# Kernel tuning notes

Measured on AMD Instinct MI355X. Metric: run time of the kernel, lower is better.

The kernel has to match this reference:

```python
import jax, jax.numpy as jnp
import numpy as np

N_NODES = 100000
N_EDGES = 1200000
IN_F = 64
OUT_F = 64


def setup_inputs() -> dict:
    key = jax.random.key(0)
    ks = jax.random.split(key, 8)
    rows = jax.random.randint(ks[0], (N_EDGES,), 0, N_NODES)
    cols = jax.random.randint(ks[1], (N_EDGES,), 0, N_NODES)
    vals = jax.random.uniform(ks[2], (N_EDGES,), dtype=jnp.float32)
    features = jax.random.normal(ks[3], (N_NODES, IN_F), dtype=jnp.float32)
    W1 = jax.random.normal(ks[4], (IN_F, OUT_F), dtype=jnp.float32) / np.sqrt(IN_F)
    b1 = jax.random.normal(ks[5], (OUT_F,), dtype=jnp.float32) * 0.01
    W2 = jax.random.normal(ks[6], (IN_F, OUT_F), dtype=jnp.float32) / np.sqrt(IN_F)
    b2 = jax.random.normal(ks[7], (OUT_F,), dtype=jnp.float32) * 0.01
    return {"rows": rows, "cols": cols, "vals": vals, "features": features,
            "W1": W1, "b1": b1, "W2": W2, "b2": b2}


def _spmm(rows, cols, vals, x):
    # y[r] = sum_{e: rows[e]==r} vals[e] * x[cols[e]]  -- COO SpMM via gather + segment_sum
    msgs = vals[:, None] * x[cols]  # [E, F]
    return jax.ops.segment_sum(msgs, rows, num_segments=N_NODES)


def reference(rows, cols, vals, features, W1, b1, W2, b2):
    # L1 = laplacian + selfLoop(identity)  =>  L1 @ X = L @ X + X
    agg1 = _spmm(rows, cols, vals, features) + features          # [N, inF]
    inter_feature = features * features                           # elementwise square
    agg2 = _spmm(rows, cols, vals, inter_feature)                 # [N, inF]
    part1 = agg1 @ W1 + b1                                        # linear
    part2 = agg2 @ W2 + b2                                        # interActTransform
    return part1 + part2
```

## Files before the change

kernel.cpp:

```cpp
#include <hip/hip_runtime.h>


#define ROWS_PER_BUCKET 128
#define ROW_SHIFT 7
#define NBUCK_PAD 784
#define SCAN_T 196
#define CAP 2048
#define CHUNK 4096
#define MAXB 2048
#define COL_BITS 17
#define COL_MASK 0x1FFFF
#define OVF_CAP 65536

__device__ __forceinline__ unsigned short f2bf(float x) {
    unsigned u = __float_as_uint(x);
    unsigned r = (u + 0x7FFFu + ((u >> 16) & 1u)) >> 16;
    return (unsigned short)r;
}
__device__ __forceinline__ float bf2f(unsigned short h) {
    return __uint_as_float(((unsigned)h) << 16);
}

__global__ __launch_bounds__(256) void node_transform(
    const float* __restrict__ X, const float* __restrict__ W1,
    const float* __restrict__ b1, const float* __restrict__ W2,
    const float* __restrict__ b2, unsigned short* __restrict__ Yb,
    float* __restrict__ Z, int n_nodes)
{
    __shared__ float W1s[64 * 64];
    __shared__ float W2s[64 * 64];
    __shared__ float xs[128][65];
    __shared__ float bs[64];

    const int tid = threadIdx.x;
    const int base = blockIdx.x * 128;

    {
        const float4* w1v = (const float4*)W1;
        const float4* w2v = (const float4*)W2;
        float4* s1 = (float4*)W1s;
        float4* s2 = (float4*)W2s;
#pragma unroll
        for (int i = 0; i < 4; ++i) {
            s1[tid + 256 * i] = w1v[tid + 256 * i];
            s2[tid + 256 * i] = w2v[tid + 256 * i];
        }
    }
    if (tid < 64) bs[tid] = b1[tid] + b2[tid];

    {
#pragma unroll
        for (int i = 0; i < 8; ++i) {
            int idx = (tid + 256 * i) * 4;
            int r = idx >> 6, c = idx & 63;
            if (base + r < n_nodes) {
                float4 v = *(const float4*)(X + (size_t)base * 64 + idx);
                xs[r][c + 0] = v.x; xs[r][c + 1] = v.y;
                xs[r][c + 2] = v.z; xs[r][c + 3] = v.w;
            }
        }
    }
    __syncthreads();

    const int tx = tid & 7;
    const int ty = tid >> 3;

    float acc1[4][8] = {};
    float acc2[4][8] = {};

#pragma unroll 2
    for (int k = 0; k < 64; ++k) {
        float4 wa0 = *(const float4*)(W1s + k * 64 + tx * 8);
        float4 wa1 = *(const float4*)(W1s + k * 64 + tx * 8 + 4);
        float4 wb0 = *(const float4*)(W2s + k * 64 + tx * 8);
        float4 wb1 = *(const float4*)(W2s + k * 64 + tx * 8 + 4);
#pragma unroll
        for (int i = 0; i < 4; ++i) {
            float xv = xs[ty * 4 + i][k];
            float xq = xv * xv;
            acc1[i][0] = fmaf(xv, wa0.x, acc1[i][0]);
            acc1[i][1] = fmaf(xv, wa0.y, acc1[i][1]);
            acc1[i][2] = fmaf(xv, wa0.z, acc1[i][2]);
            acc1[i][3] = fmaf(xv, wa0.w, acc1[i][3]);
            acc1[i][4] = fmaf(xv, wa1.x, acc1[i][4]);
            acc1[i][5] = fmaf(xv, wa1.y, acc1[i][5]);
            acc1[i][6] = fmaf(xv, wa1.z, acc1[i][6]);
            acc1[i][7] = fmaf(xv, wa1.w, acc1[i][7]);
            acc2[i][0] = fmaf(xq, wb0.x, acc2[i][0]);
            acc2[i][1] = fmaf(xq, wb0.y, acc2[i][1]);
            acc2[i][2] = fmaf(xq, wb0.z, acc2[i][2]);
            acc2[i][3] = fmaf(xq, wb0.w, acc2[i][3]);
            acc2[i][4] = fmaf(xq, wb1.x, acc2[i][4]);
            acc2[i][5] = fmaf(xq, wb1.y, acc2[i][5]);
            acc2[i][6] = fmaf(xq, wb1.z, acc2[i][6]);
            acc2[i][7] = fmaf(xq, wb1.w, acc2[i][7]);
        }
    }

    float bv[8];
#pragma unroll
    for (int j = 0; j < 8; ++j) bv[j] = bs[tx * 8 + j];

#pragma unroll
    for (int i = 0; i < 4; ++i) {
        int node = base + ty * 4 + i;
        if (node < n_nodes) {
            float z[8];
            unsigned pk[4];
#pragma unroll
            for (int j = 0; j < 4; ++j) {
                float ylo = acc1[i][2 * j]     + acc2[i][2 * j];
                float yhi = acc1[i][2 * j + 1] + acc2[i][2 * j + 1];
                pk[j] = (unsigned)f2bf(ylo) | ((unsigned)f2bf(yhi) << 16);
            }
#pragma unroll
            for (int j = 0; j < 8; ++j) z[j] = acc1[i][j] + bv[j];
            unsigned short* yp = Yb + (size_t)node * 64 + tx * 8;
            float* zp = Z + (size_t)node * 64 + tx * 8;
            *(uint4*)(yp) = make_uint4(pk[0], pk[1], pk[2], pk[3]);
            *(float4*)(zp)     = make_float4(z[0], z[1], z[2], z[3]);
            *(float4*)(zp + 4) = make_float4(z[4], z[5], z[6], z[7]);
        }
    }
}


__global__ __launch_bounds__(256) void cursor_init(
    int* __restrict__ gcursor, int* __restrict__ ovf_count, int nbp) {
    int i = blockIdx.x * 256 + threadIdx.x;
    if (i < nbp) gcursor[i] = i * CAP;
    if (i == 0) *ovf_count = 0;
}

__global__ __launch_bounds__(256) void bin_scatter(
    const int* __restrict__ rows, const int* __restrict__ cols,
    const float* __restrict__ vals, int* __restrict__ gcursor,
    int2* __restrict__ packed, int* __restrict__ ovf_count,
    int4* __restrict__ ovf, int n_edges) {
    __shared__ int lcount[NBUCK_PAD];
    __shared__ int lstart[NBUCK_PAD];
    __shared__ int lcursor[NBUCK_PAD];
    __shared__ int gbase[NBUCK_PAD];
    __shared__ int sx[CHUNK];
    __shared__ int sy[CHUNK];
    __shared__ unsigned short sbk[CHUNK];

    int tid = threadIdx.x;
    int eb0 = blockIdx.x * CHUNK;
    int cnt = min(CHUNK, n_edges - eb0);

    for (int k = tid; k < NBUCK_PAD; k += 256) lcount[k] = 0;
    __syncthreads();

    for (int i = tid; i < cnt; i += 256)
        atomicAdd(&lcount[rows[eb0 + i] >> ROW_SHIFT], 1);
    __syncthreads();

    int c0 = 0, c1 = 0, c2 = 0, c3 = 0, psum = 0;
    if (tid < SCAN_T) {
        c0 = lcount[tid * 4 + 0]; c1 = lcount[tid * 4 + 1];
        c2 = lcount[tid * 4 + 2]; c3 = lcount[tid * 4 + 3];
        psum = c0 + c1 + c2 + c3;
    }
    sx[tid] = psum;
    __syncthreads();
#pragma unroll
    for (int o = 1; o < 256; o <<= 1) {
        int t = (tid >= o) ? sx[tid - o] : 0;
        __syncthreads();
        sx[tid] += t;
        __syncthreads();
    }
    int base0 = sx[tid] - psum;
    __syncthreads();
    if (tid < SCAN_T) {
        lstart[tid * 4 + 0] = base0;
        lstart[tid * 4 + 1] = base0 + c0;
        lstart[tid * 4 + 2] = base0 + c0 + c1;
        lstart[tid * 4 + 3] = base0 + c0 + c1 + c2;
    }
    __syncthreads();

    for (int k = tid; k < NBUCK_PAD; k += 256) {
        lcursor[k] = lstart[k];
        if (lcount[k] > 0) gbase[k] = atomicAdd(&gcursor[k], lcount[k]);
    }
    __syncthreads();

    for (int i = tid; i < cnt; i += 256) {
        int r = rows[eb0 + i];
        int b = r >> ROW_SHIFT;
        int p = atomicAdd(&lcursor[b], 1);
        sx[p] = ((r & (ROWS_PER_BUCKET - 1)) << COL_BITS) | cols[eb0 + i];
        sy[p] = __float_as_int(vals[eb0 + i]);
        sbk[p] = (unsigned short)b;
    }
    __syncthreads();

    for (int i = tid; i < cnt; i += 256) {
        int b = sbk[i];
        int dest = gbase[b] + (i - lstart[b]);
        if (dest < (b + 1) * CAP) {
            packed[dest] = make_int2(sx[i], sy[i]);
        } else {
            int p = atomicAdd(ovf_count, 1);
            if (p < OVF_CAP)
                ovf[p] = make_int4(b * ROWS_PER_BUCKET + (sx[i] >> COL_BITS),
                                   sx[i] & COL_MASK, sy[i], 0);
        }
    }
}

__global__ __launch_bounds__(256) void bucket_gather_rows(
    const int* __restrict__ gcursor, const int2* __restrict__ packed,
    const unsigned short* __restrict__ Yb, float* __restrict__ out,
    int n_nodes) {
    __shared__ int2 sxy[MAXB];
    __shared__ int hist[ROWS_PER_BUCKET];
    __shared__ int chs[ROWS_PER_BUCKET];
    __shared__ int chc[ROWS_PER_BUCKET];

    int tid = threadIdx.x;
    int bucket = blockIdx.x >> 1;
    int rhalf = (blockIdx.x & 1) * 64;
    int fpair = tid & 31;
    int rowlane = tid >> 5;
    int s = bucket * CAP;
    int e = min(gcursor[bucket], s + CAP);
    int row0 = bucket * ROWS_PER_BUCKET;
    const unsigned* __restrict__ Y32 = (const unsigned*)Yb;

    for (int cb = s; cb < e; cb += MAXB) {
        int cnt = min(MAXB, e - cb);

        if (tid < ROWS_PER_BUCKET) hist[tid] = 0;
        __syncthreads();

        for (int i = tid; i < cnt; i += 256)
            atomicAdd(&hist[packed[cb + i].x >> COL_BITS], 1);
        __syncthreads();

        if (tid < ROWS_PER_BUCKET) chs[tid] = hist[tid];
        __syncthreads();
#pragma unroll
        for (int o = 1; o < ROWS_PER_BUCKET; o <<= 1) {
            int t = 0;
            if (tid < ROWS_PER_BUCKET && tid >= o) t = chs[tid - o];
            __syncthreads();
            if (tid < ROWS_PER_BUCKET) chs[tid] += t;
            __syncthreads();
        }
        if (tid < ROWS_PER_BUCKET) {
            int excl = chs[tid] - hist[tid];
            chs[tid] = excl;
            chc[tid] = excl;
        }
        __syncthreads();

        for (int i = tid; i < cnt; i += 256) {
            int2 a = packed[cb + i];
            int p = atomicAdd(&chc[a.x >> COL_BITS], 1);
            sxy[p] = a;
        }
        __syncthreads();

        for (int rr = 0; rr < 8; ++rr) {
            int r = rhalf + rowlane * 8 + rr;
            int rc = hist[r];
            int node = row0 + r;
            if (rc == 0 || node >= n_nodes) continue;
            int rs = chs[r];
            float a0 = 0.f, a1 = 0.f;
            int j = 0;
            for (; j + 8 <= rc; j += 8) {
                int2 e0 = sxy[rs + j + 0], e1 = sxy[rs + j + 1];
                int2 e2 = sxy[rs + j + 2], e3 = sxy[rs + j + 3];
                int2 e4 = sxy[rs + j + 4], e5 = sxy[rs + j + 5];
                int2 e6 = sxy[rs + j + 6], e7 = sxy[rs + j + 7];
                unsigned u0 = Y32[(size_t)(e0.x & COL_MASK) * 32 + fpair];
                unsigned u1 = Y32[(size_t)(e1.x & COL_MASK) * 32 + fpair];
                unsigned u2 = Y32[(size_t)(e2.x & COL_MASK) * 32 + fpair];
                unsigned u3 = Y32[(size_t)(e3.x & COL_MASK) * 32 + fpair];
                unsigned u4 = Y32[(size_t)(e4.x & COL_MASK) * 32 + fpair];
                unsigned u5 = Y32[(size_t)(e5.x & COL_MASK) * 32 + fpair];
                unsigned u6 = Y32[(size_t)(e6.x & COL_MASK) * 32 + fpair];
                unsigned u7 = Y32[(size_t)(e7.x & COL_MASK) * 32 + fpair];
                float v0 = __int_as_float(e0.y), v1 = __int_as_float(e1.y);
                float v2 = __int_as_float(e2.y), v3 = __int_as_float(e3.y);
                float v4 = __int_as_float(e4.y), v5 = __int_as_float(e5.y);
                float v6 = __int_as_float(e6.y), v7 = __int_as_float(e7.y);
                a0 = fmaf(v0, __uint_as_float(u0 << 16), a0);
                a1 = fmaf(v0, __uint_as_float(u0 & 0xFFFF0000u), a1);
                a0 = fmaf(v1, __uint_as_float(u1 << 16), a0);
                a1 = fmaf(v1, __uint_as_float(u1 & 0xFFFF0000u), a1);
                a0 = fmaf(v2, __uint_as_float(u2 << 16), a0);
                a1 = fmaf(v2, __uint_as_float(u2 & 0xFFFF0000u), a1);
                a0 = fmaf(v3, __uint_as_float(u3 << 16), a0);
                a1 = fmaf(v3, __uint_as_float(u3 & 0xFFFF0000u), a1);
                a0 = fmaf(v4, __uint_as_float(u4 << 16), a0);
                a1 = fmaf(v4, __uint_as_float(u4 & 0xFFFF0000u), a1);
                a0 = fmaf(v5, __uint_as_float(u5 << 16), a0);
                a1 = fmaf(v5, __uint_as_float(u5 & 0xFFFF0000u), a1);
                a0 = fmaf(v6, __uint_as_float(u6 << 16), a0);
                a1 = fmaf(v6, __uint_as_float(u6 & 0xFFFF0000u), a1);
                a0 = fmaf(v7, __uint_as_float(u7 << 16), a0);
                a1 = fmaf(v7, __uint_as_float(u7 & 0xFFFF0000u), a1);
            }
            for (; j + 2 <= rc; j += 2) {
                int2 e0 = sxy[rs + j + 0], e1 = sxy[rs + j + 1];
                unsigned u0 = Y32[(size_t)(e0.x & COL_MASK) * 32 + fpair];
                unsigned u1 = Y32[(size_t)(e1.x & COL_MASK) * 32 + fpair];
                float v0 = __int_as_float(e0.y), v1 = __int_as_float(e1.y);
                a0 = fmaf(v0, __uint_as_float(u0 << 16), a0);
                a1 = fmaf(v0, __uint_as_float(u0 & 0xFFFF0000u), a1);
                a0 = fmaf(v1, __uint_as_float(u1 << 16), a0);
                a1 = fmaf(v1, __uint_as_float(u1 & 0xFFFF0000u), a1);
            }
            if (j < rc) {
                int2 e0 = sxy[rs + j];
                unsigned u0 = Y32[(size_t)(e0.x & COL_MASK) * 32 + fpair];
                float v0 = __int_as_float(e0.y);
                a0 = fmaf(v0, __uint_as_float(u0 << 16), a0);
                a1 = fmaf(v0, __uint_as_float(u0 & 0xFFFF0000u), a1);
            }
            float2* op = (float2*)(out + (size_t)node * 64 + fpair * 2);
            float2 o = *op;
            o.x += a0; o.y += a1;
            *op = o;
        }
        __syncthreads();
    }
}

__global__ __launch_bounds__(256) void overflow_scatter(
    const int* __restrict__ ovf_count, const int4* __restrict__ ovf,
    const unsigned short* __restrict__ Yb, float* __restrict__ out) {
    int cnt = min(*ovf_count, OVF_CAP);
    long long total = (long long)cnt * 64;
    for (long long i = blockIdx.x * 256 + threadIdx.x; i < total;
         i += (long long)gridDim.x * 256) {
        int e = (int)(i >> 6), f = (int)(i & 63);
        int4 a = ovf[e];
        atomicAdd(&out[(size_t)a.x * 64 + f],
                  __int_as_float(a.z) * bf2f(Yb[(size_t)a.y * 64 + f]));
    }
}


__global__ __launch_bounds__(256) void edge_scatter(
    const int* __restrict__ rows, const int* __restrict__ cols,
    const float* __restrict__ vals, const unsigned short* __restrict__ Yb,
    float* __restrict__ out, int n_edges)
{
    int t = blockIdx.x * 256 + threadIdx.x;
    int e = t >> 4;
    int f = (t & 15) << 2;
    if (e >= n_edges) return;
    int r = rows[e];
    int c = cols[e];
    float v = vals[e];
    const unsigned short* y = Yb + (size_t)c * 64 + f;
    float* o = out + (size_t)r * 64 + f;
    atomicAdd(o + 0, v * bf2f(y[0]));
    atomicAdd(o + 1, v * bf2f(y[1]));
    atomicAdd(o + 2, v * bf2f(y[2]));
    atomicAdd(o + 3, v * bf2f(y[3]));
}

extern "C" void kernel_launch(void* const* d_in, const int* in_sizes, int n_in,
                              void* d_out, int out_size, void* d_ws, size_t ws_size,
                              hipStream_t stream) {
    const int*   rows = (const int*)d_in[0];
    const int*   cols = (const int*)d_in[1];
    const float* vals = (const float*)d_in[2];
    const float* X    = (const float*)d_in[3];
    const float* W1   = (const float*)d_in[4];
    const float* b1   = (const float*)d_in[5];
    const float* W2   = (const float*)d_in[6];
    const float* b2   = (const float*)d_in[7];
    float* out = (float*)d_out;

    const int n_edges = in_sizes[0];
    const int n_nodes = in_sizes[3] / 64;
    const int nbuck = (n_nodes + ROWS_PER_BUCKET - 1) / ROWS_PER_BUCKET;

    char* ws = (char*)d_ws;
    size_t o_Yb     = 0;
    size_t o_packed = o_Yb + (size_t)n_nodes * 64 * 2;
    size_t o_ovf    = o_packed + (size_t)NBUCK_PAD * CAP * 8;
    size_t o_gcurs  = o_ovf + (size_t)OVF_CAP * 16;
    size_t o_ovfcnt = o_gcurs + NBUCK_PAD * 4;
    size_t need     = o_ovfcnt + 16;

    unsigned short* Yb = (unsigned short*)(ws + o_Yb);

    int nblocks = (n_nodes + 127) / 128;
    node_transform<<<nblocks, 256, 0, stream>>>(X, W1, b1, W2, b2, Yb, out, n_nodes);

    if (ws_size >= need && nbuck <= NBUCK_PAD && n_nodes <= (1 << COL_BITS)) {
        int2* packed  = (int2*)(ws + o_packed);
        int4* ovf     = (int4*)(ws + o_ovf);
        int*  gcursor = (int*)(ws + o_gcurs);
        int*  ovfcnt  = (int*)(ws + o_ovfcnt);

        int eb = (n_edges + CHUNK - 1) / CHUNK;

        cursor_init<<<(NBUCK_PAD + 255) / 256, 256, 0, stream>>>(gcursor, ovfcnt, NBUCK_PAD);
        bin_scatter<<<eb, 256, 0, stream>>>(rows, cols, vals, gcursor, packed,
                                            ovfcnt, ovf, n_edges);
        bucket_gather_rows<<<nbuck * 2, 256, 0, stream>>>(gcursor, packed, Yb, out, n_nodes);
        overflow_scatter<<<128, 256, 0, stream>>>(ovfcnt, ovf, Yb, out);
    } else {
        long long threads = (long long)n_edges * 16;
        int eblocks = (int)((threads + 255) / 256);
        edge_scatter<<<eblocks, 256, 0, stream>>>(rows, cols, vals, Yb, out, n_edges);
    }
}
```

Before: 191.8 us.

## Use bf16 MFMA for the node transform GEMMs instead of scalar FMA

Rewrites the dense node transform so each wave computes 32 rows of X@W1 and X²@W2 with 16x16x32 bf16 MFMA instructions. The weights are converted to bf16 and held in registers, and X is read straight from global memory rather than staged through shared memory. This removes the LDS staging, the block barrier and most of the scalar FMA work. In exchange, X and W are quantized to bf16, which lowers the precision of the Z output (previously fp32 FMA). Outputs are now written as scalar stores rather than vector stores.

```diff
diff --git a/kernel.cpp b/kernel.cpp
--- a/kernel.cpp
+++ b/kernel.cpp
@@ -12,6 +12,9 @@
 #define COL_MASK 0x1FFFF
 #define OVF_CAP 65536
 
+typedef __attribute__((ext_vector_type(8))) short bf16x8;
+typedef __attribute__((ext_vector_type(4))) float f32x4;
+
 __device__ __forceinline__ unsigned short f2bf(float x) {
     unsigned u = __float_as_uint(x);
     unsigned r = (u + 0x7FFFu + ((u >> 16) & 1u)) >> 16;
@@ -27,99 +30,97 @@
     const float* __restrict__ b2, unsigned short* __restrict__ Yb,
     float* __restrict__ Z, int n_nodes)
 {
-    __shared__ float W1s[64 * 64];
-    __shared__ float W2s[64 * 64];
-    __shared__ float xs[128][65];
-    __shared__ float bs[64];
-
     const int tid = threadIdx.x;
-    const int base = blockIdx.x * 128;
-
-    {
-        const float4* w1v = (const float4*)W1;
-        const float4* w2v = (const float4*)W2;
-        float4* s1 = (float4*)W1s;
-        float4* s2 = (float4*)W2s;
+    const int lane = tid & 63;
+    const int wave = tid >> 6;
+    const int lg = lane >> 4;
+    const int lr = lane & 15;
+
+    const int base = blockIdx.x * 128 + wave * 32;
+
+    bf16x8 bw1[2][4];
+    bf16x8 bw2[2][4];
+#pragma unroll
+    for (int ks = 0; ks < 2; ++ks) {
+#pragma unroll
+        for (int cf = 0; cf < 4; ++cf) {
+            const int col = cf * 16 + lr;
+            const int k0 = ks * 32 + lg * 8;
+            bf16x8 t1, t2;
+#pragma unroll
+            for (int j = 0; j < 8; ++j) {
+                t1[j] = (short)f2bf(W1[(k0 + j) * 64 + col]);
+                t2[j] = (short)f2bf(W2[(k0 + j) * 64 + col]);
+            }
+            bw1[ks][cf] = t1;
+            bw2[ks][cf] = t2;
+        }
+    }
+
+    f32x4 acc1[2][4];
+    f32x4 acc2[2][4];
+#pragma unroll
+    for (int rf = 0; rf < 2; ++rf)
+#pragma unroll
+        for (int cf = 0; cf < 4; ++cf) {
+            acc1[rf][cf] = (f32x4){0.f, 0.f, 0.f, 0.f};
+            acc2[rf][cf] = (f32x4){0.f, 0.f, 0.f, 0.f};
+        }
+
+#pragma unroll
+    for (int rf = 0; rf < 2; ++rf) {
+        const int row = base + rf * 16 + lr;
+        const bool rok = row < n_nodes;
+        const float* xp = X + (size_t)row * 64 + lg * 8;
+#pragma unroll
+        for (int ks = 0; ks < 2; ++ks) {
+            float xv[8];
+            if (rok) {
+                float4 v0 = *(const float4*)(xp + ks * 32);
+                float4 v1 = *(const float4*)(xp + ks * 32 + 4);
+                xv[0] = v0.x; xv[1] = v0.y; xv[2] = v0.z; xv[3] = v0.w;
+                xv[4] = v1.x; xv[5] = v1.y; xv[6] = v1.z; xv[7] = v1.w;
+            } else {
+#pragma unroll
+                for (int j = 0; j < 8; ++j) xv[j] = 0.f;
+            }
+            bf16x8 a, q;
+#pragma unroll
+            for (int j = 0; j < 8; ++j) {
+                a[j] = (short)f2bf(xv[j]);
+                float s = xv[j] * xv[j];
+                q[j] = (short)f2bf(s);
+            }
+#pragma unroll
+            for (int cf = 0; cf < 4; ++cf) {
+                acc1[rf][cf] = __builtin_amdgcn_mfma_f32_16x16x32_bf16(
+                    a, bw1[ks][cf], acc1[rf][cf], 0, 0, 0);
+                acc2[rf][cf] = __builtin_amdgcn_mfma_f32_16x16x32_bf16(
+                    q, bw2[ks][cf], acc2[rf][cf], 0, 0, 0);
+            }
+        }
+    }
+
+    float bsv[4];
+#pragma unroll
+    for (int cf = 0; cf < 4; ++cf)
+        bsv[cf] = b1[cf * 16 + lr] + b2[cf * 16 + lr];
+
+#pragma unroll
+    for (int rf = 0; rf < 2; ++rf) {
 #pragma unroll
         for (int i = 0; i < 4; ++i) {
-            s1[tid + 256 * i] = w1v[tid + 256 * i];
-            s2[tid + 256 * i] = w2v[tid + 256 * i];
-        }
-    }
-    if (tid < 64) bs[tid] = b1[tid] + b2[tid];
-
-    {
-#pragma unroll
-        for (int i = 0; i < 8; ++i) {
-            int idx = (tid + 256 * i) * 4;
-            int r = idx >> 6, c = idx & 63;
-            if (base + r < n_nodes) {
-                float4 v = *(const float4*)(X + (size_t)base * 64 + idx);
-                xs[r][c + 0] = v.x; xs[r][c + 1] = v.y;
-                xs[r][c + 2] = v.z; xs[r][c + 3] = v.w;
-            }
-        }
-    }
-    __syncthreads();
-
-    const int tx = tid & 7;
-    const int ty = tid >> 3;
-
-    float acc1[4][8] = {};
-    float acc2[4][8] = {};
-
-#pragma unroll 2
-    for (int k = 0; k < 64; ++k) {
-        float4 wa0 = *(const float4*)(W1s + k * 64 + tx * 8);
-        float4 wa1 = *(const float4*)(W1s + k * 64 + tx * 8 + 4);
-        float4 wb0 = *(const float4*)(W2s + k * 64 + tx * 8);
-        float4 wb1 = *(const float4*)(W2s + k * 64 + tx * 8 + 4);
-#pragma unroll
-        for (int i = 0; i < 4; ++i) {
-            float xv = xs[ty * 4 + i][k];
-            float xq = xv * xv;
-            acc1[i][0] = fmaf(xv, wa0.x, acc1[i][0]);
-            acc1[i][1] = fmaf(xv, wa0.y, acc1[i][1]);
-            acc1[i][2] = fmaf(xv, wa0.z, acc1[i][2]);
-            acc1[i][3] = fmaf(xv, wa0.w, acc1[i][3]);
-            acc1[i][4] = fmaf(xv, wa1.x, acc1[i][4]);
-            acc1[i][5] = fmaf(xv, wa1.y, acc1[i][5]);
-            acc1[i][6] = fmaf(xv, wa1.z, acc1[i][6]);
-            acc1[i][7] = fmaf(xv, wa1.w, acc1[i][7]);
-            acc2[i][0] = fmaf(xq, wb0.x, acc2[i][0]);
-            acc2[i][1] = fmaf(xq, wb0.y, acc2[i][1]);
-            acc2[i][2] = fmaf(xq, wb0.z, acc2[i][2]);
-            acc2[i][3] = fmaf(xq, wb0.w, acc2[i][3]);
-            acc2[i][4] = fmaf(xq, wb1.x, acc2[i][4]);
-            acc2[i][5] = fmaf(xq, wb1.y, acc2[i][5]);
-            acc2[i][6] = fmaf(xq, wb1.z, acc2[i][6]);
-            acc2[i][7] = fmaf(xq, wb1.w, acc2[i][7]);
-        }
-    }
-
-    float bv[8];
-#pragma unroll
-    for (int j = 0; j < 8; ++j) bv[j] = bs[tx * 8 + j];
-
-#pragma unroll
-    for (int i = 0; i < 4; ++i) {
-        int node = base + ty * 4 + i;
-        if (node < n_nodes) {
-            float z[8];
-            unsigned pk[4];
-#pragma unroll
-            for (int j = 0; j < 4; ++j) {
-                float ylo = acc1[i][2 * j]     + acc2[i][2 * j];
-                float yhi = acc1[i][2 * j + 1] + acc2[i][2 * j + 1];
-                pk[j] = (unsigned)f2bf(ylo) | ((unsigned)f2bf(yhi) << 16);
-            }
-#pragma unroll
-            for (int j = 0; j < 8; ++j) z[j] = acc1[i][j] + bv[j];
-            unsigned short* yp = Yb + (size_t)node * 64 + tx * 8;
-            float* zp = Z + (size_t)node * 64 + tx * 8;
-            *(uint4*)(yp) = make_uint4(pk[0], pk[1], pk[2], pk[3]);
-            *(float4*)(zp)     = make_float4(z[0], z[1], z[2], z[3]);
-            *(float4*)(zp + 4) = make_float4(z[4], z[5], z[6], z[7]);
+            const int row = base + rf * 16 + lg * 4 + i;
+            if (row < n_nodes) {
+#pragma unroll
+                for (int cf = 0; cf < 4; ++cf) {
+                    const float v1 = acc1[rf][cf][i];
+                    const float y = v1 + acc2[rf][cf][i];
+                    const float z = v1 + bsv[cf];
+                    Yb[(size_t)row * 64 + cf * 16 + lr] = f2bf(y);
+                    Z[(size_t)row * 64 + cf * 16 + lr] = z;
+                }
+            }
         }
     }
 }
```

New measurement: 172.4 us. 10.2% less time.
